# Optimization experiments

Measured on AMD Instinct MI355X. Metric: run time of the kernel, lower is better.

Reference implementation:

```python
import jax, jax.numpy as jnp
import numpy as np

C = 64           # out_channels
DAMPENING = 0.9  # dampening_factor buffer
SUPPORT = 1.0    # pseudo_derivative_support buffer


@jax.custom_vjp
def spike(v):
    return (v > 0).astype(v.dtype)

def _spike_fwd(v):
    return spike(v), v

def _spike_bwd(v, g):
    # pseudo-derivative: dampening * max(0, 1 - |v|/support)
    pd = DAMPENING * jnp.maximum(0.0, 1.0 - jnp.abs(v) / SUPPORT)
    return (g * pd,)

spike.defvjp(_spike_fwd, _spike_bwd)


def conv2d_same(x, w, b):
    # x: (B, Cin, H, W), w: (Cout, Cin, kh, kw)
    y = jax.lax.conv_general_dilated(
        x, w, window_strides=(1, 1), padding='SAME',
        dimension_numbers=('NCHW', 'OIHW', 'NCHW'))
    return y + b[None, :, None, None]


def setup_inputs() -> dict:
    key = jax.random.key(0)
    k = jax.random.split(key, 5)
    T, B, H, W = 10, 4, 64, 64
    xt = jax.random.normal(k[0], (T, B, 3 * C, H, W), dtype=jnp.float32)
    fan_rz = C * 9
    fan_f = C * 9
    w_rz = jax.random.normal(k[1], (2 * C + 1, C, 3, 3), jnp.float32) / np.sqrt(fan_rz)
    b_rz = jax.random.normal(k[2], (2 * C + 1,), jnp.float32) * 0.01
    w_f = jax.random.normal(k[3], (C, C, 3, 3), jnp.float32) / np.sqrt(fan_f)
    b_f = jax.random.normal(k[4], (C,), jnp.float32) * 0.01
    return {'xt': xt, 'w_rz': w_rz, 'b_rz': b_rz, 'w_f': w_f, 'b_f': b_f, 'stage': 0}


def reference(xt, w_rz, b_rz, w_f, b_f, stage):
    T, B, _, H, W = xt.shape
    prev_y0 = jnp.zeros((B, C, H, W), jnp.float32)
    h0 = jnp.zeros((B, C, H, W), jnp.float32)

    def step(carry, xi):
        prev_y, h = carry
        xi_z, xi_r, xi_f = jnp.split(xi, 3, axis=1)          # each (B,C,H,W)
        rz = conv2d_same(prev_y, w_rz, b_rz)                 # (B, 2C+1, H, W)
        z = rz[:, :C]
        r = rz[:, C:2 * C]
        thr_logit = rz[:, 2 * C:2 * C + 1]                   # (B,1,H,W)
        update_gate = jax.nn.sigmoid(z + xi_z)
        reset_gate = jax.nn.sigmoid(r + xi_r)
        f = conv2d_same(prev_y * reset_gate, w_f, b_f) + xi_f
        input_gate = jnp.tanh(f)
        h = (1.0 - update_gate) * h + update_gate * input_gate
        thr = jax.nn.sigmoid(thr_logit)
        d = h - thr
        event = spike(d)
        neg_dist = jnp.where(d < 0, thr - h, 0.0)
        y = h * event
        h_new = h - event * thr
        return (y, h_new), (y, event, neg_dist)

    _, (ys, events, neg_dists) = jax.lax.scan(step, (prev_y0, h0), xt)
    return ys, events, neg_dists
```

## Files before the change

### kernel.cpp

```cpp
#include <hip/hip_runtime.h>
#include <math.h>

#define CC 64
#define HW 4096
#define NB 4
#define NT 10
#define TR 4
#define CHUNK 16
#define LDSROW 68
#define ICSTRIDE (6*LDSROW)
#define BUFSZ (CHUNK*ICSTRIDE)

__device__ __forceinline__ float sigm(float x) { return 1.0f / (1.0f + expf(-x)); }

__device__ __forceinline__ void load_win6(const float* __restrict__ p, float (&w)[3][6]) {
#pragma unroll
    for (int dr = 0; dr < 3; ++dr) {
        float4 a  = *(const float4*)(p + dr * LDSROW);
        float2 e2 = *(const float2*)(p + dr * LDSROW + 4);
        w[dr][0] = a.x;  w[dr][1] = a.y;  w[dr][2] = a.z;
        w[dr][3] = a.w;  w[dr][4] = e2.x; w[dr][5] = e2.y;
    }
}

__device__ __forceinline__ void fma36(const float* __restrict__ w9,
                                      const float (&win)[3][6], float (&a)[4]) {
    float w0=w9[0],w1=w9[1],w2=w9[2],w3=w9[3],w4=w9[4];
    float w5=w9[5],w6=w9[6],w7=w9[7],w8=w9[8];
#pragma unroll
    for (int pp = 0; pp < 4; ++pp) {
        float s = a[pp];
        s = fmaf(w0, win[0][pp],   s);
        s = fmaf(w1, win[0][pp+1], s);
        s = fmaf(w2, win[0][pp+2], s);
        s = fmaf(w3, win[1][pp],   s);
        s = fmaf(w4, win[1][pp+1], s);
        s = fmaf(w5, win[1][pp+2], s);
        s = fmaf(w6, win[2][pp],   s);
        s = fmaf(w7, win[2][pp+1], s);
        s = fmaf(w8, win[2][pp+2], s);
        a[pp] = s;
    }
}

__global__ __launch_bounds__(512, 2) void convA_kernel(
    const float* __restrict__ prev_y,
    const float* __restrict__ xt_t,
    const float* __restrict__ w_rz,
    const float* __restrict__ b_rz,
    float* __restrict__ ws_u,
    float* __restrict__ ws_ry,
    float* __restrict__ ws_thr,
    int first)
{
    __shared__ float lds[2 * BUFSZ];
    const int tid = threadIdx.x;
    const int tx  = tid & 15;
    const int t4  = (tid >> 4) & 3;
    const int ocq = tid >> 6;
    const int b   = blockIdx.x;
    const int r0  = blockIdx.y * TR;
    const int ocg = blockIdx.z;
    const int oc0 = __builtin_amdgcn_readfirstlane(ocg * 32 + ocq * 4);
    const bool do_thr = (ocg == 0) && (ocq == 0);

    float acc[4][4];
#pragma unroll
    for (int o = 0; o < 4; ++o)
#pragma unroll
        for (int p = 0; p < 4; ++p) acc[o][p] = 0.f;
    float acct[4] = {0.f, 0.f, 0.f, 0.f};

    if (!first) {
        const int q   = tid & 15;
        const int icl = (tid >> 4) & 15;
        const int rh  = tid >> 8;
        const float* gsrc = prev_y + ((size_t)b * CC + icl) * HW;
        float4 pf[3];

#pragma unroll
        for (int j = 0; j < 3; ++j) {
            int sr = r0 - 1 + rh * 3 + j;
            pf[j] = make_float4(0.f, 0.f, 0.f, 0.f);
            if (sr >= 0 && sr < 64)
                pf[j] = *(const float4*)(gsrc + sr * 64 + 4 * q);
        }
        {
            float* dst = lds + icl * ICSTRIDE;
#pragma unroll
            for (int j = 0; j < 3; ++j) {
                int row = rh * 3 + j;
                float aw = __shfl_up(pf[j].w, 1, 16);
                if (q == 0) aw = 0.f;
                *(float4*)(dst + row * LDSROW + 4 * q) =
                    make_float4(aw, pf[j].x, pf[j].y, pf[j].z);
                if (q == 15)
                    *(float4*)(dst + row * LDSROW + 64) =
                        make_float4(pf[j].w, 0.f, 0.f, 0.f);
            }
        }
        __syncthreads();

#pragma unroll 1
        for (int ck = 0; ck < 4; ++ck) {
            if (ck < 3) {
                const float* g = gsrc + (size_t)(ck + 1) * CHUNK * HW;
#pragma unroll
                for (int j = 0; j < 3; ++j) {
                    int sr = r0 - 1 + rh * 3 + j;
                    pf[j] = make_float4(0.f, 0.f, 0.f, 0.f);
                    if (sr >= 0 && sr < 64)
                        pf[j] = *(const float4*)(g + sr * 64 + 4 * q);
                }
            }
            const float* p  = lds + (ck & 1) * BUFSZ + t4 * LDSROW + 4 * tx;
            const float* wz = w_rz + ((size_t)oc0 * CC + ck * CHUNK) * 9;
            const float* wt = w_rz + ((size_t)128 * CC + ck * CHUNK) * 9;
#pragma unroll 1
            for (int ic = 0; ic < CHUNK; ++ic) {
                float win[3][6];
                load_win6(p, win);
                fma36(wz,              win, acc[0]);
                fma36(wz + 1 * CC * 9, win, acc[1]);
                fma36(wz + 2 * CC * 9, win, acc[2]);
                fma36(wz + 3 * CC * 9, win, acc[3]);
                if (do_thr) fma36(wt, win, acct);
                p  += ICSTRIDE;
                wz += 9;
                wt += 9;
            }
            if (ck < 3) {
                float* dst = lds + ((ck + 1) & 1) * BUFSZ + icl * ICSTRIDE;
#pragma unroll
                for (int j = 0; j < 3; ++j) {
                    int row = rh * 3 + j;
                    float aw = __shfl_up(pf[j].w, 1, 16);
                    if (q == 0) aw = 0.f;
                    *(float4*)(dst + row * LDSROW + 4 * q) =
                        make_float4(aw, pf[j].x, pf[j].y, pf[j].z);
                    if (q == 15)
                        *(float4*)(dst + row * LDSROW + 64) =
                            make_float4(pf[j].w, 0.f, 0.f, 0.f);
                }
            }
            __syncthreads();
        }
    }

    const int gr = r0 + t4;
    const size_t pix = (size_t)gr * 64 + 4 * tx;
    if (ocg < 2) {
#pragma unroll
        for (int o = 0; o < 4; ++o) {
            int oc = oc0 + o;
            float bias = b_rz[oc];
            const float4 x4 = *(const float4*)(xt_t + ((size_t)b * 192 + oc) * HW + pix);
            float4 outv;
            outv.x = sigm(acc[o][0] + bias + x4.x);
            outv.y = sigm(acc[o][1] + bias + x4.y);
            outv.z = sigm(acc[o][2] + bias + x4.z);
            outv.w = sigm(acc[o][3] + bias + x4.w);
            *(float4*)(ws_u + ((size_t)b * CC + oc) * HW + pix) = outv;
        }
    } else {
#pragma unroll
        for (int o = 0; o < 4; ++o) {
            int oc = oc0 + o;
            int ch = oc - CC;
            float bias = b_rz[oc];
            const float4 x4 = *(const float4*)(xt_t + ((size_t)b * 192 + oc) * HW + pix);
            float4 py;
            if (first) { py = make_float4(0.f, 0.f, 0.f, 0.f); }
            else       { py = *(const float4*)(prev_y + ((size_t)b * CC + ch) * HW + pix); }
            float4 outv;
            outv.x = py.x * sigm(acc[o][0] + bias + x4.x);
            outv.y = py.y * sigm(acc[o][1] + bias + x4.y);
            outv.z = py.z * sigm(acc[o][2] + bias + x4.z);
            outv.w = py.w * sigm(acc[o][3] + bias + x4.w);
            *(float4*)(ws_ry + ((size_t)b * CC + ch) * HW + pix) = outv;
        }
    }
    if (do_thr) {
        float bias = b_rz[2 * CC];
        float4 outv;
        outv.x = sigm(acct[0] + bias);
        outv.y = sigm(acct[1] + bias);
        outv.z = sigm(acct[2] + bias);
        outv.w = sigm(acct[3] + bias);
        *(float4*)(ws_thr + (size_t)b * HW + pix) = outv;
    }
}

__global__ __launch_bounds__(256, 2) void convB_kernel(
    const float* __restrict__ ry,
    const float* __restrict__ xt_t,
    const float* __restrict__ w_f,
    const float* __restrict__ b_f,
    const float* __restrict__ ws_u,
    const float* __restrict__ ws_thr,
    float* __restrict__ ws_h,
    float* __restrict__ out_y,
    float* __restrict__ out_e,
    float* __restrict__ out_nd,
    int first)
{
    __shared__ float lds[2 * BUFSZ];
    const int tid = threadIdx.x;
    const int tx  = tid & 15;
    const int t4  = (tid >> 4) & 3;
    const int ocq = tid >> 6;
    const int b   = blockIdx.x;
    const int r0  = blockIdx.y * TR;
    const int ocg = blockIdx.z;
    const int oc0 = __builtin_amdgcn_readfirstlane(ocg * 16 + ocq * 4);

    float acc[4][4];
#pragma unroll
    for (int o = 0; o < 4; ++o)
#pragma unroll
        for (int p = 0; p < 4; ++p) acc[o][p] = 0.f;

    if (!first) {
        const int q   = tid & 15;
        const int icl = (tid >> 4) & 15;
        const float* gsrc = ry + ((size_t)b * CC + icl) * HW;
        float4 pf[6];

#pragma unroll
        for (int j = 0; j < 6; ++j) {
            int sr = r0 - 1 + j;
            pf[j] = make_float4(0.f, 0.f, 0.f, 0.f);
            if (sr >= 0 && sr < 64)
                pf[j] = *(const float4*)(gsrc + sr * 64 + 4 * q);
        }
        {
            float* dst = lds + icl * ICSTRIDE;
#pragma unroll
            for (int j = 0; j < 6; ++j) {
                float aw = __shfl_up(pf[j].w, 1, 16);
                if (q == 0) aw = 0.f;
                *(float4*)(dst + j * LDSROW + 4 * q) =
                    make_float4(aw, pf[j].x, pf[j].y, pf[j].z);
                if (q == 15)
                    *(float4*)(dst + j * LDSROW + 64) =
                        make_float4(pf[j].w, 0.f, 0.f, 0.f);
            }
        }
        __syncthreads();

#pragma unroll 1
        for (int ck = 0; ck < 4; ++ck) {
            if (ck < 3) {
                const float* g = gsrc + (size_t)(ck + 1) * CHUNK * HW;
#pragma unroll
                for (int j = 0; j < 6; ++j) {
                    int sr = r0 - 1 + j;
                    pf[j] = make_float4(0.f, 0.f, 0.f, 0.f);
                    if (sr >= 0 && sr < 64)
                        pf[j] = *(const float4*)(g + sr * 64 + 4 * q);
                }
            }
            const float* p  = lds + (ck & 1) * BUFSZ + t4 * LDSROW + 4 * tx;
            const float* wb = w_f + ((size_t)oc0 * CC + ck * CHUNK) * 9;
            float winA[3][6], winB[3][6];
            load_win6(p, winA);
#pragma unroll 1
            for (int ic2 = 0; ic2 < CHUNK; ic2 += 2) {
                load_win6(p + ICSTRIDE, winB);
                fma36(wb,              winA, acc[0]);
                fma36(wb + 1 * CC * 9, winA, acc[1]);
                fma36(wb + 2 * CC * 9, winA, acc[2]);
                fma36(wb + 3 * CC * 9, winA, acc[3]);
                if (ic2 + 2 < CHUNK)
                    load_win6(p + 2 * ICSTRIDE, winA);
                fma36(wb + 9,              winB, acc[0]);
                fma36(wb + 9 + 1 * CC * 9, winB, acc[1]);
                fma36(wb + 9 + 2 * CC * 9, winB, acc[2]);
                fma36(wb + 9 + 3 * CC * 9, winB, acc[3]);
                p  += 2 * ICSTRIDE;
                wb += 18;
            }
            if (ck < 3) {
                float* dst = lds + ((ck + 1) & 1) * BUFSZ + icl * ICSTRIDE;
#pragma unroll
                for (int j = 0; j < 6; ++j) {
                    float aw = __shfl_up(pf[j].w, 1, 16);
                    if (q == 0) aw = 0.f;
                    *(float4*)(dst + j * LDSROW + 4 * q) =
                        make_float4(aw, pf[j].x, pf[j].y, pf[j].z);
                    if (q == 15)
                        *(float4*)(dst + j * LDSROW + 64) =
                            make_float4(pf[j].w, 0.f, 0.f, 0.f);
                }
            }
            __syncthreads();
        }
    }

    const int gr = r0 + t4;
    const size_t pix = (size_t)gr * 64 + 4 * tx;
    const float4 t4q = *(const float4*)(ws_thr + (size_t)b * HW + pix);
#pragma unroll
    for (int o = 0; o < 4; ++o) {
        int oc = oc0 + o;
        float bias = b_f[oc];
        const size_t coff = ((size_t)b * CC + oc) * HW + pix;
        const float4 x4 = *(const float4*)(xt_t + ((size_t)b * 192 + 2 * CC + oc) * HW + pix);
        const float4 u4 = *(const float4*)(ws_u + coff);
        float4 h4;
        if (first) { h4 = make_float4(0.f, 0.f, 0.f, 0.f); }
        else       { h4 = *(const float4*)(ws_h + coff); }

        float fx[4] = { acc[o][0] + bias + x4.x, acc[o][1] + bias + x4.y,
                        acc[o][2] + bias + x4.z, acc[o][3] + bias + x4.w };
        float uu[4] = { u4.x, u4.y, u4.z, u4.w };
        float hh[4] = { h4.x, h4.y, h4.z, h4.w };
        float tt[4] = { t4q.x, t4q.y, t4q.z, t4q.w };
        float yv[4], ev[4], nd[4], hc[4];
#pragma unroll
        for (int j = 0; j < 4; ++j) {
            float ig = tanhf(fx[j]);
            float hn = (1.f - uu[j]) * hh[j] + uu[j] * ig;
            float d  = hn - tt[j];
            bool pos = d > 0.f;
            ev[j] = pos ? 1.f : 0.f;
            yv[j] = pos ? hn : 0.f;
            nd[j] = (d < 0.f) ? (tt[j] - hn) : 0.f;
            hc[j] = pos ? (hn - tt[j]) : hn;
        }
        *(float4*)(out_y + coff)  = make_float4(yv[0], yv[1], yv[2], yv[3]);
        *(float4*)(out_e + coff)  = make_float4(ev[0], ev[1], ev[2], ev[3]);
        *(float4*)(out_nd + coff) = make_float4(nd[0], nd[1], nd[2], nd[3]);
        *(float4*)(ws_h + coff)   = make_float4(hc[0], hc[1], hc[2], hc[3]);
    }
}

extern "C" void kernel_launch(void* const* d_in, const int* in_sizes, int n_in,
                              void* d_out, int out_size, void* d_ws, size_t ws_size,
                              hipStream_t stream) {
    const float* xt   = (const float*)d_in[0];
    const float* w_rz = (const float*)d_in[1];
    const float* b_rz = (const float*)d_in[2];
    const float* w_f  = (const float*)d_in[3];
    const float* b_f  = (const float*)d_in[4];
    float* out = (float*)d_out;
    float* ws  = (float*)d_ws;

    const size_t NCHW = (size_t)NB * CC * HW;
    float* ws_u   = ws;
    float* ws_ry  = ws + NCHW;
    float* ws_thr = ws + 2 * NCHW;
    float* ws_h   = ws + 2 * NCHW + (size_t)NB * HW;

    float* ys  = out;
    float* es  = out + (size_t)NT * NCHW;
    float* nds = out + 2 * (size_t)NT * NCHW;

    for (int t = 0; t < NT; ++t) {
        const float* xtt = xt + (size_t)t * NB * 192 * HW;
        const float* py  = (t == 0) ? xtt : (ys + (size_t)(t - 1) * NCHW);
        hipLaunchKernelGGL(convA_kernel, dim3(NB, 16, 4), dim3(512), 0, stream,
                           py, xtt, w_rz, b_rz, ws_u, ws_ry, ws_thr, (t == 0) ? 1 : 0);
        hipLaunchKernelGGL(convB_kernel, dim3(NB, 16, 4), dim3(256), 0, stream,
                           ws_ry, xtt, w_f, b_f, ws_u, ws_thr, ws_h,
                           ys + (size_t)t * NCHW, es + (size_t)t * NCHW,
                           nds + (size_t)t * NCHW, (t == 0) ? 1 : 0);
    }
}
```

Before: 1.054 ms.

## Double-buffer convA LDS window loads and widen convB to 512 threads

convA's inner channel loop is unrolled by two and uses ping-pong window registers, so the next input channel's LDS window load overlaps the current FMAs, as convB already did. convB now runs 512 threads per block, with each thread computing 2 output channels instead of 4 and loading 3 halo rows instead of 6. This gives more waves per block to hide latency, at the cost of less register-level weight/window reuse per thread. ocq now spans 8 groups of 2 channels, which still covers 16 channels per block.

```diff
diff --git a/kernel.cpp b/kernel.cpp
--- a/kernel.cpp
+++ b/kernel.cpp
@@ -116,18 +116,27 @@
             const float* p  = lds + (ck & 1) * BUFSZ + t4 * LDSROW + 4 * tx;
             const float* wz = w_rz + ((size_t)oc0 * CC + ck * CHUNK) * 9;
             const float* wt = w_rz + ((size_t)128 * CC + ck * CHUNK) * 9;
+
+            float winA[3][6], winB[3][6];
+            load_win6(p, winA);
 #pragma unroll 1
-            for (int ic = 0; ic < CHUNK; ++ic) {
-                float win[3][6];
-                load_win6(p, win);
-                fma36(wz,              win, acc[0]);
-                fma36(wz + 1 * CC * 9, win, acc[1]);
-                fma36(wz + 2 * CC * 9, win, acc[2]);
-                fma36(wz + 3 * CC * 9, win, acc[3]);
-                if (do_thr) fma36(wt, win, acct);
-                p  += ICSTRIDE;
-                wz += 9;
-                wt += 9;
+            for (int ic2 = 0; ic2 < CHUNK; ic2 += 2) {
+                load_win6(p + ICSTRIDE, winB);
+                fma36(wz,              winA, acc[0]);
+                fma36(wz + 1 * CC * 9, winA, acc[1]);
+                fma36(wz + 2 * CC * 9, winA, acc[2]);
+                fma36(wz + 3 * CC * 9, winA, acc[3]);
+                if (do_thr) fma36(wt, winA, acct);
+                if (ic2 + 2 < CHUNK)
+                    load_win6(p + 2 * ICSTRIDE, winA);
+                fma36(wz + 9,              winB, acc[0]);
+                fma36(wz + 9 + 1 * CC * 9, winB, acc[1]);
+                fma36(wz + 9 + 2 * CC * 9, winB, acc[2]);
+                fma36(wz + 9 + 3 * CC * 9, winB, acc[3]);
+                if (do_thr) fma36(wt + 9, winB, acct);
+                p  += 2 * ICSTRIDE;
+                wz += 18;
+                wt += 18;
             }
             if (ck < 3) {
                 float* dst = lds + ((ck + 1) & 1) * BUFSZ + icl * ICSTRIDE;
@@ -191,7 +200,7 @@
     }
 }
 
-__global__ __launch_bounds__(256, 2) void convB_kernel(
+__global__ __launch_bounds__(512, 2) void convB_kernel(
     const float* __restrict__ ry,
     const float* __restrict__ xt_t,
     const float* __restrict__ w_f,
@@ -212,23 +221,24 @@
     const int b   = blockIdx.x;
     const int r0  = blockIdx.y * TR;
     const int ocg = blockIdx.z;
-    const int oc0 = __builtin_amdgcn_readfirstlane(ocg * 16 + ocq * 4);
-
-    float acc[4][4];
-#pragma unroll
-    for (int o = 0; o < 4; ++o)
+    const int oc0 = __builtin_amdgcn_readfirstlane(ocg * 16 + ocq * 2);
+
+    float acc[2][4];
+#pragma unroll
+    for (int o = 0; o < 2; ++o)
 #pragma unroll
         for (int p = 0; p < 4; ++p) acc[o][p] = 0.f;
 
     if (!first) {
         const int q   = tid & 15;
         const int icl = (tid >> 4) & 15;
+        const int rh  = tid >> 8;
         const float* gsrc = ry + ((size_t)b * CC + icl) * HW;
-        float4 pf[6];
-
-#pragma unroll
-        for (int j = 0; j < 6; ++j) {
-            int sr = r0 - 1 + j;
+        float4 pf[3];
+
+#pragma unroll
+        for (int j = 0; j < 3; ++j) {
+            int sr = r0 - 1 + rh * 3 + j;
             pf[j] = make_float4(0.f, 0.f, 0.f, 0.f);
             if (sr >= 0 && sr < 64)
                 pf[j] = *(const float4*)(gsrc + sr * 64 + 4 * q);
@@ -236,13 +246,14 @@
         {
             float* dst = lds + icl * ICSTRIDE;
 #pragma unroll
-            for (int j = 0; j < 6; ++j) {
+            for (int j = 0; j < 3; ++j) {
+                int row = rh * 3 + j;
                 float aw = __shfl_up(pf[j].w, 1, 16);
                 if (q == 0) aw = 0.f;
-                *(float4*)(dst + j * LDSROW + 4 * q) =
+                *(float4*)(dst + row * LDSROW + 4 * q) =
                     make_float4(aw, pf[j].x, pf[j].y, pf[j].z);
                 if (q == 15)
-                    *(float4*)(dst + j * LDSROW + 64) =
+                    *(float4*)(dst + row * LDSROW + 64) =
                         make_float4(pf[j].w, 0.f, 0.f, 0.f);
             }
         }
@@ -253,8 +264,8 @@
             if (ck < 3) {
                 const float* g = gsrc + (size_t)(ck + 1) * CHUNK * HW;
 #pragma unroll
-                for (int j = 0; j < 6; ++j) {
-                    int sr = r0 - 1 + j;
+                for (int j = 0; j < 3; ++j) {
+                    int sr = r0 - 1 + rh * 3 + j;
                     pf[j] = make_float4(0.f, 0.f, 0.f, 0.f);
                     if (sr >= 0 && sr < 64)
                         pf[j] = *(const float4*)(g + sr * 64 + 4 * q);
@@ -262,34 +273,32 @@
             }
             const float* p  = lds + (ck & 1) * BUFSZ + t4 * LDSROW + 4 * tx;
             const float* wb = w_f + ((size_t)oc0 * CC + ck * CHUNK) * 9;
+
             float winA[3][6], winB[3][6];
             load_win6(p, winA);
 #pragma unroll 1
             for (int ic2 = 0; ic2 < CHUNK; ic2 += 2) {
                 load_win6(p + ICSTRIDE, winB);
-                fma36(wb,              winA, acc[0]);
-                fma36(wb + 1 * CC * 9, winA, acc[1]);
-                fma36(wb + 2 * CC * 9, winA, acc[2]);
-                fma36(wb + 3 * CC * 9, winA, acc[3]);
+                fma36(wb,          winA, acc[0]);
+                fma36(wb + CC * 9, winA, acc[1]);
                 if (ic2 + 2 < CHUNK)
                     load_win6(p + 2 * ICSTRIDE, winA);
-                fma36(wb + 9,              winB, acc[0]);
-                fma36(wb + 9 + 1 * CC * 9, winB, acc[1]);
-                fma36(wb + 9 + 2 * CC * 9, winB, acc[2]);
-                fma36(wb + 9 + 3 * CC * 9, winB, acc[3]);
+                fma36(wb + 9,          winB, acc[0]);
+                fma36(wb + 9 + CC * 9, winB, acc[1]);
                 p  += 2 * ICSTRIDE;
                 wb += 18;
             }
             if (ck < 3) {
                 float* dst = lds + ((ck + 1) & 1) * BUFSZ + icl * ICSTRIDE;
 #pragma unroll
-                for (int j = 0; j < 6; ++j) {
+                for (int j = 0; j < 3; ++j) {
+                    int row = rh * 3 + j;
                     float aw = __shfl_up(pf[j].w, 1, 16);
                     if (q == 0) aw = 0.f;
-                    *(float4*)(dst + j * LDSROW + 4 * q) =
+                    *(float4*)(dst + row * LDSROW + 4 * q) =
                         make_float4(aw, pf[j].x, pf[j].y, pf[j].z);
                     if (q == 15)
-                        *(float4*)(dst + j * LDSROW + 64) =
+                        *(float4*)(dst + row * LDSROW + 64) =
                             make_float4(pf[j].w, 0.f, 0.f, 0.f);
                 }
             }
@@ -301,7 +310,7 @@
     const size_t pix = (size_t)gr * 64 + 4 * tx;
     const float4 t4q = *(const float4*)(ws_thr + (size_t)b * HW + pix);
 #pragma unroll
-    for (int o = 0; o < 4; ++o) {
+    for (int o = 0; o < 2; ++o) {
         int oc = oc0 + o;
         float bias = b_f[oc];
         const size_t coff = ((size_t)b * CC + oc) * HW + pix;
@@ -361,7 +370,7 @@
         const float* py  = (t == 0) ? xtt : (ys + (size_t)(t - 1) * NCHW);
         hipLaunchKernelGGL(convA_kernel, dim3(NB, 16, 4), dim3(512), 0, stream,
                            py, xtt, w_rz, b_rz, ws_u, ws_ry, ws_thr, (t == 0) ? 1 : 0);
-        hipLaunchKernelGGL(convB_kernel, dim3(NB, 16, 4), dim3(256), 0, stream,
+        hipLaunchKernelGGL(convB_kernel, dim3(NB, 16, 4), dim3(512), 0, stream,
                            ws_ry, xtt, w_f, b_f, ws_u, ws_thr, ws_h,
                            ys + (size_t)t * NCHW, es + (size_t)t * NCHW,
                            nds + (size_t)t * NCHW, (t == 0) ? 1 : 0);
```

Measured after the change: 921.6 us. 1.14x faster.
